# Kernel optimization log

Hardware: AMD Instinct MI355X
Metric: run time of the kernel (lower is better)

## Reference

```python
import jax, jax.numpy as jnp
import numpy as np

B, S, P, I = 32, 64, 32, 256
NF, H, L = 4, 512, 2
OUT = 2
INITRANGE = 0.1
assert NF * I == 2 * H  # layer-2 GRU input dim equals layer-1 input dim


def setup_inputs() -> dict:
    key = jax.random.key(0)
    ks = jax.random.split(key, 12)
    u = lambda k, shape: jax.random.uniform(k, shape, jnp.float32, -INITRANGE, INITRANGE)
    return {
        "inputs": jax.random.normal(ks[0], (B, S, P, I), jnp.float32),
        "inputs_demoip": jax.random.normal(ks[1], (B, 3), jnp.float32),
        "conv_w": u(ks[2], (NF, I)),            # Conv1d(1, NF, kernel=I) == dot product
        "conv_b": u(ks[3], (NF,)),
        "conv2_w": u(ks[4], (2 * H,)),          # Conv1d(1, 1, kernel=2H) == dot product
        "conv2_b": u(ks[5], (1,)),
        "wih": u(ks[6], (L, 2, 3 * H, NF * I)),  # [layer, dir, 3H, in]
        "whh": u(ks[7], (L, 2, 3 * H, H)),
        "bih": u(ks[8], (L, 2, 3 * H)),
        "bhh": u(ks[9], (L, 2, 3 * H)),
        "lin_w": u(ks[10], (OUT, 2 * H + 3)),
        "lin_b": u(ks[11], (OUT,)),
        "batch_size": B,
    }


def _gru_dir(x, wih, whh, bih, bhh, reverse):
    """One direction of a torch-style GRU. x: [B,S,in] -> [B,S,H]."""
    gx = jnp.einsum('bsi,gi->bsg', x, wih) + bih  # precompute input gates [B,S,3H]
    if reverse:
        gx = gx[:, ::-1]
    h0 = jnp.zeros((x.shape[0], H), x.dtype)

    def step(h, gxt):
        gh = h @ whh.T + bhh
        xr, xz, xn = jnp.split(gxt, 3, axis=-1)
        hr, hz, hn = jnp.split(gh, 3, axis=-1)
        r = jax.nn.sigmoid(xr + hr)
        z = jax.nn.sigmoid(xz + hz)
        n = jnp.tanh(xn + r * hn)
        h_new = (1.0 - z) * n + z * h
        return h_new, h_new

    _, ys = jax.lax.scan(step, h0, gx.transpose(1, 0, 2))
    ys = ys.transpose(1, 0, 2)  # [B,S,H]
    if reverse:
        ys = ys[:, ::-1]
    return ys


def reference(inputs, inputs_demoip, conv_w, conv_b, conv2_w, conv2_b,
              wih, whh, bih, bhh, lin_w, lin_b, batch_size):
    # --- convolutional attention embedding (kernel spans full input -> dot product) ---
    scores = jnp.einsum('bspi,fi->bsfp', inputs, conv_w) + conv_b[None, None, :, None]
    conv_wts = jax.nn.softmax(scores, axis=-1)                    # softmax over pad dim
    vec = jnp.einsum('bsfp,bspi->bsfi', conv_wts, inputs)         # [B,S,NF,I]
    embedding = vec.reshape(batch_size, S, NF * I)                # [B,S,NF*I]

    # --- stacked bidirectional GRU (eval mode: dropout omitted) ---
    x = embedding
    for l in range(L):
        f = _gru_dir(x, wih[l, 0], whh[l, 0], bih[l, 0], bhh[l, 0], False)
        b = _gru_dir(x, wih[l, 1], whh[l, 1], bih[l, 1], bhh[l, 1], True)
        x = jnp.concatenate([f, b], axis=-1)
    states = x                                                    # [B,S,2H]

    # --- second attention (conv2 kernel spans 2H -> dot product per step) ---
    alpha = jax.nn.softmax(states @ conv2_w + conv2_b[0], axis=1)  # [B,S]
    context = jnp.einsum('bs,bsh->bh', alpha, states)              # [B,2H]

    context_v2 = jnp.concatenate([context, inputs_demoip], axis=1)  # [B,2H+3]
    out = jax.nn.softmax(context_v2 @ lin_w.T + lin_b, axis=1)      # [B,OUT]
    return out, conv_wts, states, context, alpha
```

## Files before the change

kernel.cpp:

```cpp
#include <hip/hip_runtime.h>

typedef __attribute__((ext_vector_type(8))) short s8v;
typedef __attribute__((ext_vector_type(8))) __bf16 bf8v;
typedef __attribute__((ext_vector_type(4))) float f32x4;
typedef unsigned long long ULL;

#define DEVINL __device__ __forceinline__

DEVINL unsigned short f2bf(float f) {
    unsigned int x = __float_as_uint(f);
    unsigned int r = (x + 0x7FFFu + ((x >> 16) & 1u)) >> 16;
    return (unsigned short)r;
}

DEVINL f32x4 mfma16(s8v a, s8v b, f32x4 c) {
    return __builtin_amdgcn_mfma_f32_16x16x32_bf16(
        __builtin_bit_cast(bf8v, a), __builtin_bit_cast(bf8v, b), c, 0, 0, 0);
}

#define WS_FLAGS 0
#define WS_HBUF  8192
#define WS_ZERO_BYTES 270336
#define WS_WIH   270336
#define WS_WHH   (WS_WIH + 12582912)
#define WS_EMB   (WS_WHH + 6291456)
#define WS_ST1   (WS_EMB + 4194304)
#define WS_GX    (WS_ST1 + 4194304)

__global__ __launch_bounds__(256) void k_cvt(const float* __restrict__ in,
                                             unsigned short* __restrict__ out, int n) {
    int i0 = (blockIdx.x * 256 + threadIdx.x) * 8;
    if (i0 + 8 > n) return;
    f32x4 a = *(const f32x4*)(in + i0);
    f32x4 b = *(const f32x4*)(in + i0 + 4);
    s8v o;
    o[0] = (short)f2bf(a[0]); o[1] = (short)f2bf(a[1]);
    o[2] = (short)f2bf(a[2]); o[3] = (short)f2bf(a[3]);
    o[4] = (short)f2bf(b[0]); o[5] = (short)f2bf(b[1]);
    o[6] = (short)f2bf(b[2]); o[7] = (short)f2bf(b[3]);
    *(s8v*)(out + i0) = o;
}

__global__ __launch_bounds__(256) void k_conv(const float* __restrict__ inp,
                                              const float* __restrict__ conv_w,
                                              const float* __restrict__ conv_b,
                                              float* __restrict__ wts_out,
                                              unsigned short* __restrict__ emb) {
    const int bs = blockIdx.x, tid = threadIdx.x;
    __shared__ float xs[32][260];
    __shared__ float sc[4][32];
    __shared__ float wts[4][32];
    const float* x = inp + (size_t)bs * 8192;
    {
        int p = tid >> 3, i0 = (tid & 7) * 32;
        const float* src = x + p * 256 + i0;
        float* dst = &xs[p][i0];
#pragma unroll
        for (int j = 0; j < 32; j += 4) *(f32x4*)(dst + j) = *(const f32x4*)(src + j);
    }
    __syncthreads();
    {
        int p = tid >> 3, o = tid & 7;
        float s0 = 0, s1 = 0, s2 = 0, s3 = 0;
        const float* xp = &xs[p][o * 32];
#pragma unroll
        for (int j = 0; j < 32; j += 4) {
            f32x4 v  = *(const f32x4*)(xp + j);
            f32x4 w0 = *(const f32x4*)(conv_w + o * 32 + j);
            f32x4 w1 = *(const f32x4*)(conv_w + 256 + o * 32 + j);
            f32x4 w2 = *(const f32x4*)(conv_w + 512 + o * 32 + j);
            f32x4 w3 = *(const f32x4*)(conv_w + 768 + o * 32 + j);
#pragma unroll
            for (int q = 0; q < 4; ++q) {
                s0 += v[q] * w0[q]; s1 += v[q] * w1[q];
                s2 += v[q] * w2[q]; s3 += v[q] * w3[q];
            }
        }
#pragma unroll
        for (int d = 4; d; d >>= 1) {
            s0 += __shfl_down(s0, d, 8); s1 += __shfl_down(s1, d, 8);
            s2 += __shfl_down(s2, d, 8); s3 += __shfl_down(s3, d, 8);
        }
        if (o == 0) {
            sc[0][p] = s0 + conv_b[0]; sc[1][p] = s1 + conv_b[1];
            sc[2][p] = s2 + conv_b[2]; sc[3][p] = s3 + conv_b[3];
        }
    }
    __syncthreads();
    if (tid < 4) {
        float mx = -1e30f;
        for (int p = 0; p < 32; ++p) mx = fmaxf(mx, sc[tid][p]);
        float sm = 0.f;
        for (int p = 0; p < 32; ++p) { float e = __expf(sc[tid][p] - mx); wts[tid][p] = e; sm += e; }
        float inv = 1.f / sm;
        for (int p = 0; p < 32; ++p) wts[tid][p] *= inv;
    }
    __syncthreads();
    if (tid < 128) wts_out[(size_t)bs * 128 + tid] = wts[tid >> 5][tid & 31];
    {
        float a0 = 0, a1 = 0, a2 = 0, a3 = 0;
#pragma unroll 8
        for (int p = 0; p < 32; ++p) {
            float v = xs[p][tid];
            a0 += wts[0][p] * v; a1 += wts[1][p] * v;
            a2 += wts[2][p] * v; a3 += wts[3][p] * v;
        }
        unsigned short* e = emb + (size_t)bs * 1024;
        e[tid] = f2bf(a0); e[256 + tid] = f2bf(a1);
        e[512 + tid] = f2bf(a2); e[768 + tid] = f2bf(a3);
    }
}

__global__ __launch_bounds__(256, 2) void k_gemm(const unsigned short* __restrict__ A,
                                                 const unsigned short* __restrict__ B,
                                                 const float* __restrict__ bias,
                                                 float* __restrict__ C,
                                                 int M, int N, int K) {
    const int bm = blockIdx.y * 64, bn = blockIdx.x * 64;
    const int tid = threadIdx.x, w = tid >> 6, l = tid & 63;
    const int wm = (w >> 1) * 32, wn = (w & 1) * 32;
    __shared__ unsigned short As[64][72];
    __shared__ unsigned short Bs[64][72];
    f32x4 acc[2][2] = {};
    const int sr = tid >> 2;
    const int sk = (tid & 3) * 8;
    const int am = (l & 15), ak = (l >> 4) * 8;
    for (int k0 = 0; k0 < K; k0 += 64) {
        s8v a0 = *(const s8v*)(A + (size_t)(bm + sr) * K + k0 + sk);
        s8v a1 = *(const s8v*)(A + (size_t)(bm + sr) * K + k0 + sk + 32);
        s8v b0 = *(const s8v*)(B + (size_t)(bn + sr) * K + k0 + sk);
        s8v b1 = *(const s8v*)(B + (size_t)(bn + sr) * K + k0 + sk + 32);
        __syncthreads();
        *(s8v*)&As[sr][sk] = a0; *(s8v*)&As[sr][sk + 32] = a1;
        *(s8v*)&Bs[sr][sk] = b0; *(s8v*)&Bs[sr][sk + 32] = b1;
        __syncthreads();
#pragma unroll
        for (int kk = 0; kk < 64; kk += 32) {
            s8v fa0 = *(const s8v*)&As[wm + am][kk + ak];
            s8v fa1 = *(const s8v*)&As[wm + 16 + am][kk + ak];
            s8v fb0 = *(const s8v*)&Bs[wn + am][kk + ak];
            s8v fb1 = *(const s8v*)&Bs[wn + 16 + am][kk + ak];
            acc[0][0] = mfma16(fa0, fb0, acc[0][0]);
            acc[0][1] = mfma16(fa0, fb1, acc[0][1]);
            acc[1][0] = mfma16(fa1, fb0, acc[1][0]);
            acc[1][1] = mfma16(fa1, fb1, acc[1][1]);
        }
    }
#pragma unroll
    for (int mt = 0; mt < 2; ++mt)
#pragma unroll
        for (int nt = 0; nt < 2; ++nt)
#pragma unroll
            for (int r = 0; r < 4; ++r) {
                int row = bm + wm + mt * 16 + (l >> 4) * 4 + r;
                int col = bn + wn + nt * 16 + (l & 15);
                C[(size_t)row * N + col] = acc[mt][nt][r] + bias[col];
            }
}

#define STEP(T, PGC, PGN)                                                         \
  {                                                                               \
    const int t_ = (T);                                                           \
    const int s_ = dir ? (63 - t_) : t_;                                          \
    if (t_ > 0 && l < 32) {                                                       \
      while (__hip_atomic_load(&fl[l * 16], __ATOMIC_RELAXED,                     \
                               __HIP_MEMORY_SCOPE_AGENT) < (unsigned)t_)          \
        __builtin_amdgcn_s_sleep(1);                                              \
    }                                                                             \
    {                                                                             \
      const ULL* hc = (const ULL*)(hb0 + (size_t)(t_ & 1) * 16384);               \
      _Pragma("unroll") for (int i = 0; i < 8; ++i) {                             \
        const int c = tid + 256 * i;                                              \
        const int row = c >> 6, ch = c & 63;                                      \
        ULL d0 = __hip_atomic_load(hc + row * 128 + ch * 2, __ATOMIC_RELAXED,     \
                                   __HIP_MEMORY_SCOPE_AGENT);                     \
        ULL d1 = __hip_atomic_load(hc + row * 128 + ch * 2 + 1, __ATOMIC_RELAXED, \
                                   __HIP_MEMORY_SCOPE_AGENT);                     \
        unsigned short* dst = &hs[t_ & 1][row][ch * 8];                           \
        *(ULL*)dst = d0;                                                          \
        *(ULL*)(dst + 4) = d1;                                                    \
      }                                                                           \
    }                                                                             \
    __syncthreads();                                                              \
    f32x4 acc[3][2] = {};                                                         \
    _Pragma("unroll") for (int bt = 0; bt < 2; ++bt) {                            \
      const unsigned short* hrow = &hs[t_ & 1][bt * 16 + lr][lq * 8];             \
      _Pragma("unroll") for (int kt = 0; kt < 16; ++kt) {                         \
        s8v hf = *(const s8v*)(hrow + kt * 32);                                   \
        acc[0][bt] = mfma16(bf[0][kt], hf, acc[0][bt]);                           \
        acc[1][bt] = mfma16(bf[1][kt], hf, acc[1][bt]);                           \
        acc[2][bt] = mfma16(bf[2][kt], hf, acc[2][bt]);                           \
      }                                                                           \
    }                                                                             \
    unsigned short* hnw = hb0 + (size_t)((t_ + 1) & 1) * 16384;                   \
    float4 hn4[2];                                                                \
    ULL pks[2];                                                                   \
    _Pragma("unroll") for (int bt = 0; bt < 2; ++bt) {                            \
      ULL pk = 0;                                                                 \
      _Pragma("unroll") for (int r = 0; r < 4; ++r) {                             \
        float xr = ((const float*)&(PGC)[0][bt])[r];                              \
        float xz = ((const float*)&(PGC)[1][bt])[r];                              \
        float xn = ((const float*)&(PGC)[2][bt])[r];                              \
        float r_ = __builtin_amdgcn_rcpf(                                         \
            1.f + __expf(-(xr + acc[0][bt][r] + ((const float*)&bh4[0])[r])));    \
        float z_ = __builtin_amdgcn_rcpf(                                         \
            1.f + __expf(-(xz + acc[1][bt][r] + ((const float*)&bh4[1])[r])));    \
        float q = xn + r_ * (acc[2][bt][r] + ((const float*)&bh4[2])[r]);         \
        q = fminf(fmaxf(q, -15.f), 15.f);                                         \
        float e = __expf(2.f * q);                                                \
        float n_ = (e - 1.f) * __builtin_amdgcn_rcpf(e + 1.f);                    \
        float h = (1.f - z_) * n_ + z_ * hp[bt][r];                               \
        hp[bt][r] = h;                                                            \
        ((float*)&hn4[bt])[r] = h;                                                \
        pk |= (ULL)f2bf(h) << (16 * r);                                           \
      }                                                                           \
      pks[bt] = pk;                                                               \
      __hip_atomic_store((ULL*)hnw + (bt * 16 + lr) * 128 + (col4 >> 2), pk,      \
                         __ATOMIC_RELAXED, __HIP_MEMORY_SCOPE_AGENT);             \
    }                                                                             \
    asm volatile("s_waitcnt vmcnt(0)" ::: "memory");                              \
    if (l == 0 && t_ < 63)                                                        \
      __hip_atomic_store(myflag, (unsigned)(t_ + 1), __ATOMIC_RELAXED,            \
                         __HIP_MEMORY_SCOPE_AGENT);                               \
    if (t_ < 63) {                                                                \
      const int sn = dir ? (62 - t_) : (t_ + 1);                                  \
      _Pragma("unroll") for (int g = 0; g < 3; ++g)                               \
        _Pragma("unroll") for (int bt = 0; bt < 2; ++bt)                          \
          (PGN)[g][bt] = *(const float4*)(gxd +                                   \
              (size_t)((bt * 16 + lr) * 64 + sn) * 3072 + g * 512 + col4);        \
    }                                                                             \
    _Pragma("unroll") for (int bt = 0; bt < 2; ++bt) {                            \
      const size_t so = (size_t)((bt * 16 + lr) * 64 + s_) * 1024 + dir * 512 + col4; \
      if (st32) *(float4*)(st32 + so) = hn4[bt];                                  \
      if (st16) *(ULL*)(st16 + so) = pks[bt];                                     \
    }                                                                             \
  }

__global__ __launch_bounds__(256, 1) void k_scan(const float* __restrict__ gx,
                                                 const unsigned short* __restrict__ whh,
                                                 const float* __restrict__ bhh,
                                                 unsigned short* __restrict__ hbuf,
                                                 unsigned int* __restrict__ flags,
                                                 float* __restrict__ st32,
                                                 unsigned short* __restrict__ st16) {
    const int blk = blockIdx.x;
    const int dir = blk >> 3, jg = blk & 7;
    const int tid = threadIdx.x;
    const int w = tid >> 6, l = tid & 63;
    const int lr = l & 15, lq = l >> 4;
    const int jb = jg * 64;
    const int colA = jb + w * 16 + lr;
    const int col4 = jb + w * 16 + lq * 4;

    __shared__ __align__(1024) unsigned short hs[2][32][520];

    s8v bf[3][16];
#pragma unroll
    for (int g = 0; g < 3; ++g) {
        const unsigned short* wr =
            whh + ((size_t)dir * 1536 + g * 512 + colA) * 512 + lq * 8;
#pragma unroll
        for (int kt = 0; kt < 16; ++kt) bf[g][kt] = *(const s8v*)(wr + kt * 32);
    }
    float4 bh4[3];
#pragma unroll
    for (int g = 0; g < 3; ++g)
        bh4[g] = *(const float4*)(bhh + dir * 1536 + g * 512 + col4);

    unsigned short* hb0 = hbuf + (size_t)dir * 32768;
    unsigned int* fl = flags + dir * 512;
    unsigned int* myflag = fl + (jg * 4 + w) * 16;
    const float* gxd = gx + dir * 1536;

    float hp[2][4] = {{0.f, 0.f, 0.f, 0.f}, {0.f, 0.f, 0.f, 0.f}};
    float4 pgA[3][2], pgB[3][2];
    {
        const int s0 = dir ? 63 : 0;
#pragma unroll
        for (int g = 0; g < 3; ++g)
#pragma unroll
            for (int bt = 0; bt < 2; ++bt)
                pgA[g][bt] = *(const float4*)(gxd +
                    (size_t)((bt * 16 + lr) * 64 + s0) * 3072 + g * 512 + col4);
    }

    for (int tt = 0; tt < 64; tt += 2) {
        STEP(tt, pgA, pgB)
        STEP(tt + 1, pgB, pgA)
    }
}

__global__ __launch_bounds__(256) void k_finale(const float* __restrict__ states,
                                                const float* __restrict__ conv2_w,
                                                const float* __restrict__ conv2_b,
                                                const float* __restrict__ demoip,
                                                const float* __restrict__ lin_w,
                                                const float* __restrict__ lin_b,
                                                float* __restrict__ out,
                                                float* __restrict__ context,
                                                float* __restrict__ alpha) {
    const int b = blockIdx.x, tid = threadIdx.x, w = tid >> 6, l = tid & 63;
    __shared__ float dots[64], al[64], ctx[1024], lg[2];
    const float* st = states + (size_t)b * 65536;
    for (int si = 0; si < 16; ++si) {
        int s = w * 16 + si;
        const float* row = st + s * 1024;
        float sum = 0.f;
        for (int i = l; i < 1024; i += 64) sum += row[i] * conv2_w[i];
#pragma unroll
        for (int m = 32; m; m >>= 1) sum += __shfl_xor(sum, m, 64);
        if (l == 0) dots[s] = sum + conv2_b[0];
    }
    __syncthreads();
    if (w == 0) {
        float v = dots[l];
        float mx = v;
#pragma unroll
        for (int m = 32; m; m >>= 1) mx = fmaxf(mx, __shfl_xor(mx, m, 64));
        float e = __expf(v - mx);
        float sm = e;
#pragma unroll
        for (int m = 32; m; m >>= 1) sm += __shfl_xor(sm, m, 64);
        float a = e / sm;
        al[l] = a;
        alpha[b * 64 + l] = a;
    }
    __syncthreads();
    for (int h = tid; h < 1024; h += 256) {
        float c = 0.f;
#pragma unroll 8
        for (int s = 0; s < 64; ++s) c += al[s] * st[s * 1024 + h];
        ctx[h] = c;
        context[b * 1024 + h] = c;
    }
    __syncthreads();
    if (w < 2) {
        const float* lw = lin_w + w * 1027;
        float sum = 0.f;
        for (int i = l; i < 1024; i += 64) sum += ctx[i] * lw[i];
#pragma unroll
        for (int m = 32; m; m >>= 1) sum += __shfl_xor(sum, m, 64);
        if (l == 0) {
            sum += lw[1024] * demoip[b * 3] + lw[1025] * demoip[b * 3 + 1] +
                   lw[1026] * demoip[b * 3 + 2] + lin_b[w];
            lg[w] = sum;
        }
    }
    __syncthreads();
    if (tid == 0) {
        float m = fmaxf(lg[0], lg[1]);
        float e0 = __expf(lg[0] - m), e1 = __expf(lg[1] - m);
        float inv = 1.f / (e0 + e1);
        out[b * 2 + 0] = e0 * inv;
        out[b * 2 + 1] = e1 * inv;
    }
}

extern "C" void kernel_launch(void* const* d_in, const int* in_sizes, int n_in,
                              void* d_out, int out_size, void* d_ws, size_t ws_size,
                              hipStream_t stream) {
    const float* inputs  = (const float*)d_in[0];
    const float* demoip  = (const float*)d_in[1];
    const float* conv_w  = (const float*)d_in[2];
    const float* conv_b  = (const float*)d_in[3];
    const float* conv2_w = (const float*)d_in[4];
    const float* conv2_b = (const float*)d_in[5];
    const float* wih     = (const float*)d_in[6];
    const float* whh     = (const float*)d_in[7];
    const float* bih     = (const float*)d_in[8];
    const float* bhh     = (const float*)d_in[9];
    const float* lin_w   = (const float*)d_in[10];
    const float* lin_b   = (const float*)d_in[11];

    char* ws = (char*)d_ws;
    unsigned int* flags   = (unsigned int*)(ws + WS_FLAGS);
    unsigned short* hbuf  = (unsigned short*)(ws + WS_HBUF);
    unsigned short* wih16 = (unsigned short*)(ws + WS_WIH);
    unsigned short* whh16 = (unsigned short*)(ws + WS_WHH);
    unsigned short* emb16 = (unsigned short*)(ws + WS_EMB);
    unsigned short* st116 = (unsigned short*)(ws + WS_ST1);
    float* gxbuf          = (float*)(ws + WS_GX);

    float* out_out    = (float*)d_out;
    float* wts_out    = out_out + 64;
    float* states_out = out_out + 262208;
    float* ctx_out    = out_out + 2359360;
    float* alpha_out  = out_out + 2392128;

    hipMemsetAsync(ws, 0, WS_ZERO_BYTES, stream);
    k_cvt<<<3072, 256, 0, stream>>>(wih, wih16, 6291456);
    k_cvt<<<1536, 256, 0, stream>>>(whh, whh16, 3145728);
    k_conv<<<2048, 256, 0, stream>>>(inputs, conv_w, conv_b, wts_out, emb16);
    k_gemm<<<dim3(48, 32), 256, 0, stream>>>(emb16, wih16, bih, gxbuf, 2048, 3072, 1024);
    k_scan<<<16, 256, 0, stream>>>(gxbuf, whh16, bhh, hbuf, flags, nullptr, st116);
    k_gemm<<<dim3(48, 32), 256, 0, stream>>>(st116, wih16 + 3145728, bih + 3072, gxbuf,
                                             2048, 3072, 1024);
    k_scan<<<16, 256, 0, stream>>>(gxbuf, whh16 + 1572864, bhh + 3072, hbuf + 65536,
                                   flags + 1024, states_out, nullptr);
    k_finale<<<32, 256, 0, stream>>>(states_out, conv2_w, conv2_b, demoip, lin_w, lin_b,
                                     out_out, ctx_out, alpha_out);
}
```

Before: 925.0 us.

## Replace GRU scan flag barriers with step-tagged hidden-state words and fold biases

The cross-block synchronisation in the recurrent scan drops per-wave flags and the vmcnt wait. Each hidden-state chunk is now stored as a 64-bit word whose upper half carries the timestep, so consumers poll the data itself until every tag matches and each block writes its own slice straight into LDS. The r/z recurrent biases are folded into the input-gate GEMM epilogue through a second bias pointer, leaving only the n-gate bias in the scan. This removes a store-fence-flag round trip per step, at the cost of doubling the exchange buffer size and more polling loads per thread.

```diff
diff --git a/kernel.cpp b/kernel.cpp
--- a/kernel.cpp
+++ b/kernel.cpp
@@ -18,10 +18,9 @@
         __builtin_bit_cast(bf8v, a), __builtin_bit_cast(bf8v, b), c, 0, 0, 0);
 }
 
-#define WS_FLAGS 0
-#define WS_HBUF  8192
-#define WS_ZERO_BYTES 270336
-#define WS_WIH   270336
+#define WS_HLL   0
+#define WS_ZERO_BYTES 524288
+#define WS_WIH   524288
 #define WS_WHH   (WS_WIH + 12582912)
 #define WS_EMB   (WS_WHH + 6291456)
 #define WS_ST1   (WS_EMB + 4194304)
@@ -114,6 +113,7 @@
 __global__ __launch_bounds__(256, 2) void k_gemm(const unsigned short* __restrict__ A,
                                                  const unsigned short* __restrict__ B,
                                                  const float* __restrict__ bias,
+                                                 const float* __restrict__ bias2,
                                                  float* __restrict__ C,
                                                  int M, int N, int K) {
     const int bm = blockIdx.y * 64, bn = blockIdx.x * 64;
@@ -154,7 +154,9 @@
             for (int r = 0; r < 4; ++r) {
                 int row = bm + wm + mt * 16 + (l >> 4) * 4 + r;
                 int col = bn + wn + nt * 16 + (l & 15);
-                C[(size_t)row * N + col] = acc[mt][nt][r] + bias[col];
+                int gg = col >> 9;
+                float b2 = (gg != 2 && gg != 5 && bias2) ? bias2[col] : 0.f;
+                C[(size_t)row * N + col] = acc[mt][nt][r] + bias[col] + b2;
             }
 }
 
@@ -162,29 +164,30 @@
   {                                                                               \
     const int t_ = (T);                                                           \
     const int s_ = dir ? (63 - t_) : t_;                                          \
-    if (t_ > 0 && l < 32) {                                                       \
-      while (__hip_atomic_load(&fl[l * 16], __ATOMIC_RELAXED,                     \
-                               __HIP_MEMORY_SCOPE_AGENT) < (unsigned)t_)          \
+    ULL* cur = hb + (size_t)(t_ & 1) * 8192;                                      \
+    const bool skip = (t_ > 0) && (tid >= jbc) && (tid < jbc + 32);               \
+    if (!skip) {                                                                  \
+      ULL v[32];                                                                  \
+      for (;;) {                                                                  \
+        _Pragma("unroll") for (int i = 0; i < 32; ++i)                            \
+            v[i] = __hip_atomic_load(cur + i * 256 + tid, __ATOMIC_RELAXED,       \
+                                     __HIP_MEMORY_SCOPE_AGENT);                   \
+        bool ok = true;                                                           \
+        _Pragma("unroll") for (int i = 0; i < 32; ++i)                            \
+            ok = ok && ((unsigned)(v[i] >> 32) == (unsigned)t_);                  \
+        if (ok) break;                                                            \
         __builtin_amdgcn_s_sleep(1);                                              \
-    }                                                                             \
-    {                                                                             \
-      const ULL* hc = (const ULL*)(hb0 + (size_t)(t_ & 1) * 16384);               \
-      _Pragma("unroll") for (int i = 0; i < 8; ++i) {                             \
-        const int c = tid + 256 * i;                                              \
-        const int row = c >> 6, ch = c & 63;                                      \
-        ULL d0 = __hip_atomic_load(hc + row * 128 + ch * 2, __ATOMIC_RELAXED,     \
-                                   __HIP_MEMORY_SCOPE_AGENT);                     \
-        ULL d1 = __hip_atomic_load(hc + row * 128 + ch * 2 + 1, __ATOMIC_RELAXED, \
-                                   __HIP_MEMORY_SCOPE_AGENT);                     \
-        unsigned short* dst = &hs[t_ & 1][row][ch * 8];                           \
-        *(ULL*)dst = d0;                                                          \
-        *(ULL*)(dst + 4) = d1;                                                    \
       }                                                                           \
+      _Pragma("unroll") for (int i = 0; i < 32; ++i)                              \
+          *(unsigned int*)((char*)hs + (t_ & 1) * 33280 + i * 1040 + tid * 4) =   \
+              (unsigned int)v[i];                                                 \
     }                                                                             \
     __syncthreads();                                                              \
     f32x4 acc[3][2] = {};                                                         \
     _Pragma("unroll") for (int bt = 0; bt < 2; ++bt) {                            \
-      const unsigned short* hrow = &hs[t_ & 1][bt * 16 + lr][lq * 8];             \
+      const unsigned short* hrow =                                                \
+          (const unsigned short*)((const char*)hs + (t_ & 1) * 33280 +            \
+                                  (bt * 16 + lr) * 1040) + lq * 8;                \
       _Pragma("unroll") for (int kt = 0; kt < 16; ++kt) {                         \
         s8v hf = *(const s8v*)(hrow + kt * 32);                                   \
         acc[0][bt] = mfma16(bf[0][kt], hf, acc[0][bt]);                           \
@@ -192,36 +195,42 @@
         acc[2][bt] = mfma16(bf[2][kt], hf, acc[2][bt]);                           \
       }                                                                           \
     }                                                                             \
-    unsigned short* hnw = hb0 + (size_t)((t_ + 1) & 1) * 16384;                   \
+    ULL* nxt = hb + (size_t)((t_ + 1) & 1) * 8192;                                \
     float4 hn4[2];                                                                \
-    ULL pks[2];                                                                   \
+    unsigned int dd[2][2];                                                        \
     _Pragma("unroll") for (int bt = 0; bt < 2; ++bt) {                            \
-      ULL pk = 0;                                                                 \
       _Pragma("unroll") for (int r = 0; r < 4; ++r) {                             \
         float xr = ((const float*)&(PGC)[0][bt])[r];                              \
         float xz = ((const float*)&(PGC)[1][bt])[r];                              \
         float xn = ((const float*)&(PGC)[2][bt])[r];                              \
-        float r_ = __builtin_amdgcn_rcpf(                                         \
-            1.f + __expf(-(xr + acc[0][bt][r] + ((const float*)&bh4[0])[r])));    \
-        float z_ = __builtin_amdgcn_rcpf(                                         \
-            1.f + __expf(-(xz + acc[1][bt][r] + ((const float*)&bh4[1])[r])));    \
-        float q = xn + r_ * (acc[2][bt][r] + ((const float*)&bh4[2])[r]);         \
+        float r_ = __builtin_amdgcn_rcpf(1.f + __expf(-(xr + acc[0][bt][r])));    \
+        float z_ = __builtin_amdgcn_rcpf(1.f + __expf(-(xz + acc[1][bt][r])));    \
+        float q = xn + r_ * (acc[2][bt][r] + bhN[r]);                             \
         q = fminf(fmaxf(q, -15.f), 15.f);                                         \
         float e = __expf(2.f * q);                                                \
         float n_ = (e - 1.f) * __builtin_amdgcn_rcpf(e + 1.f);                    \
         float h = (1.f - z_) * n_ + z_ * hp[bt][r];                               \
         hp[bt][r] = h;                                                            \
         ((float*)&hn4[bt])[r] = h;                                                \
-        pk |= (ULL)f2bf(h) << (16 * r);                                           \
       }                                                                           \
-      pks[bt] = pk;                                                               \
-      __hip_atomic_store((ULL*)hnw + (bt * 16 + lr) * 128 + (col4 >> 2), pk,      \
-                         __ATOMIC_RELAXED, __HIP_MEMORY_SCOPE_AGENT);             \
+      const int row_ = bt * 16 + lr;                                              \
+      dd[bt][0] = (unsigned int)f2bf(((float*)&hn4[bt])[0]) |                     \
+                  ((unsigned int)f2bf(((float*)&hn4[bt])[1]) << 16);              \
+      dd[bt][1] = (unsigned int)f2bf(((float*)&hn4[bt])[2]) |                     \
+                  ((unsigned int)f2bf(((float*)&hn4[bt])[3]) << 16);              \
+      if (t_ < 63) {                                                              \
+        __hip_atomic_store(nxt + row_ * 256 + chk,                                \
+                           (ULL)dd[bt][0] | ((ULL)(t_ + 1) << 32),                \
+                           __ATOMIC_RELAXED, __HIP_MEMORY_SCOPE_AGENT);           \
+        __hip_atomic_store(nxt + row_ * 256 + chk + 1,                            \
+                           (ULL)dd[bt][1] | ((ULL)(t_ + 1) << 32),                \
+                           __ATOMIC_RELAXED, __HIP_MEMORY_SCOPE_AGENT);           \
+      }                                                                           \
+      *(unsigned int*)((char*)hs + ((t_ + 1) & 1) * 33280 + row_ * 1040 +         \
+                       chk * 4) = dd[bt][0];                                      \
+      *(unsigned int*)((char*)hs + ((t_ + 1) & 1) * 33280 + row_ * 1040 +         \
+                       (chk + 1) * 4) = dd[bt][1];                                \
     }                                                                             \
-    asm volatile("s_waitcnt vmcnt(0)" ::: "memory");                              \
-    if (l == 0 && t_ < 63)                                                        \
-      __hip_atomic_store(myflag, (unsigned)(t_ + 1), __ATOMIC_RELAXED,            \
-                         __HIP_MEMORY_SCOPE_AGENT);                               \
     if (t_ < 63) {                                                                \
       const int sn = dir ? (62 - t_) : (t_ + 1);                                  \
       _Pragma("unroll") for (int g = 0; g < 3; ++g)                               \
@@ -232,15 +241,14 @@
     _Pragma("unroll") for (int bt = 0; bt < 2; ++bt) {                            \
       const size_t so = (size_t)((bt * 16 + lr) * 64 + s_) * 1024 + dir * 512 + col4; \
       if (st32) *(float4*)(st32 + so) = hn4[bt];                                  \
-      if (st16) *(ULL*)(st16 + so) = pks[bt];                                     \
+      if (st16) *(ULL*)(st16 + so) = (ULL)dd[bt][0] | ((ULL)dd[bt][1] << 32);     \
     }                                                                             \
   }
 
 __global__ __launch_bounds__(256, 1) void k_scan(const float* __restrict__ gx,
                                                  const unsigned short* __restrict__ whh,
                                                  const float* __restrict__ bhh,
-                                                 unsigned short* __restrict__ hbuf,
-                                                 unsigned int* __restrict__ flags,
+                                                 ULL* __restrict__ hLL,
                                                  float* __restrict__ st32,
                                                  unsigned short* __restrict__ st16) {
     const int blk = blockIdx.x;
@@ -249,8 +257,10 @@
     const int w = tid >> 6, l = tid & 63;
     const int lr = l & 15, lq = l >> 4;
     const int jb = jg * 64;
+    const int jbc = jg * 32;
     const int colA = jb + w * 16 + lr;
     const int col4 = jb + w * 16 + lq * 4;
+    const int chk = col4 >> 1;
 
     __shared__ __align__(1024) unsigned short hs[2][32][520];
 
@@ -262,14 +272,10 @@
 #pragma unroll
         for (int kt = 0; kt < 16; ++kt) bf[g][kt] = *(const s8v*)(wr + kt * 32);
     }
-    float4 bh4[3];
-#pragma unroll
-    for (int g = 0; g < 3; ++g)
-        bh4[g] = *(const float4*)(bhh + dir * 1536 + g * 512 + col4);
-
-    unsigned short* hb0 = hbuf + (size_t)dir * 32768;
-    unsigned int* fl = flags + dir * 512;
-    unsigned int* myflag = fl + (jg * 4 + w) * 16;
+    float bhN[4];
+    *(float4*)bhN = *(const float4*)(bhh + dir * 1536 + 1024 + col4);
+
+    ULL* hb = hLL + (size_t)dir * 16384;
     const float* gxd = gx + dir * 1536;
 
     float hp[2][4] = {{0.f, 0.f, 0.f, 0.f}, {0.f, 0.f, 0.f, 0.f}};
@@ -373,8 +379,8 @@
     const float* lin_b   = (const float*)d_in[11];
 
     char* ws = (char*)d_ws;
-    unsigned int* flags   = (unsigned int*)(ws + WS_FLAGS);
-    unsigned short* hbuf  = (unsigned short*)(ws + WS_HBUF);
+    ULL* hLL0             = (ULL*)(ws + WS_HLL);
+    ULL* hLL1             = hLL0 + 32768;
     unsigned short* wih16 = (unsigned short*)(ws + WS_WIH);
     unsigned short* whh16 = (unsigned short*)(ws + WS_WHH);
     unsigned short* emb16 = (unsigned short*)(ws + WS_EMB);
@@ -391,12 +397,13 @@
     k_cvt<<<3072, 256, 0, stream>>>(wih, wih16, 6291456);
     k_cvt<<<1536, 256, 0, stream>>>(whh, whh16, 3145728);
     k_conv<<<2048, 256, 0, stream>>>(inputs, conv_w, conv_b, wts_out, emb16);
-    k_gemm<<<dim3(48, 32), 256, 0, stream>>>(emb16, wih16, bih, gxbuf, 2048, 3072, 1024);
-    k_scan<<<16, 256, 0, stream>>>(gxbuf, whh16, bhh, hbuf, flags, nullptr, st116);
-    k_gemm<<<dim3(48, 32), 256, 0, stream>>>(st116, wih16 + 3145728, bih + 3072, gxbuf,
+    k_gemm<<<dim3(48, 32), 256, 0, stream>>>(emb16, wih16, bih, bhh, gxbuf,
                                              2048, 3072, 1024);
-    k_scan<<<16, 256, 0, stream>>>(gxbuf, whh16 + 1572864, bhh + 3072, hbuf + 65536,
-                                   flags + 1024, states_out, nullptr);
+    k_scan<<<16, 256, 0, stream>>>(gxbuf, whh16, bhh, hLL0, nullptr, st116);
+    k_gemm<<<dim3(48, 32), 256, 0, stream>>>(st116, wih16 + 3145728, bih + 3072,
+                                             bhh + 3072, gxbuf, 2048, 3072, 1024);
+    k_scan<<<16, 256, 0, stream>>>(gxbuf, whh16 + 1572864, bhh + 3072, hLL1,
+                                   states_out, nullptr);
     k_finale<<<32, 256, 0, stream>>>(states_out, conv2_w, conv2_b, demoip, lin_w, lin_b,
                                      out_out, ctx_out, alpha_out);
 }
```

After: 1.189 ms. 28.5% more time.
